# Optimization experiments

Hardware: AMD Instinct MI355X
Metric: run time of the kernel (lower is better)

Reference implementation:

```python
import jax, jax.numpy as jnp
import numpy as np

THRESHOLD = 0.1
EPS = 1e-06


def _bilinear_warp(img, flow):
    """Backward-warp img [B,1,H,W] by flow [B,2,H,W] with bilinear sampling,
    zero padding for out-of-range taps (F.grid_sample zeros-padding semantics)."""
    B, _, H, W = img.shape
    imgf = img[:, 0].reshape(B, H * W)                      # [B, H*W]
    ys, xs = jnp.meshgrid(jnp.arange(H, dtype=flow.dtype),
                          jnp.arange(W, dtype=flow.dtype), indexing='ij')
    x = xs[None] + flow[:, 0]                               # [B,H,W] sample x
    y = ys[None] + flow[:, 1]                               # [B,H,W] sample y
    x0 = jnp.floor(x)
    y0 = jnp.floor(y)
    wx = x - x0
    wy = y - y0
    x0i = x0.astype(jnp.int32)
    y0i = y0.astype(jnp.int32)

    def tap(xi, yi):
        inb = ((xi >= 0) & (xi < W) & (yi >= 0) & (yi < H)).astype(img.dtype)
        idx = (jnp.clip(yi, 0, H - 1) * W + jnp.clip(xi, 0, W - 1)).reshape(B, H * W)
        vals = jnp.take_along_axis(imgf, idx, axis=1).reshape(B, H, W)
        return vals * inb

    out = (tap(x0i, y0i) * (1 - wx) * (1 - wy)
           + tap(x0i + 1, y0i) * wx * (1 - wy)
           + tap(x0i, y0i + 1) * (1 - wx) * wy
           + tap(x0i + 1, y0i + 1) * wx * wy)
    return out[:, None]                                     # [B,1,H,W]


def _forward(img1, img2, flow, event_voxels, valid_mask):
    B, _, H, W = flow.shape
    C = event_voxels.shape[1]
    rgb_w = jnp.array([0.299, 0.587, 0.114], dtype=img1.dtype)
    gray1 = jnp.einsum('bchw,c->bhw', img1, rgb_w)[:, None]  # [B,1,H,W]
    gray2 = jnp.einsum('bchw,c->bhw', img2, rgb_w)[:, None]
    warped_gray2 = _bilinear_warp(gray2, flow)
    normalized_change = jnp.tanh((warped_gray2 - gray1) * 5.0)[:, 0]  # [B,H,W]
    pos = jax.nn.relu(normalized_change)
    neg = jax.nn.relu(-normalized_change)

    # pred_events: ch0=pos, ch1=neg, ch i+2 = pos*w + neg*(1-w), w=(i+1)/(C-1)
    rem = C - 2
    w = jnp.arange(1, rem + 1, dtype=pos.dtype) / (rem + 1)          # [rem]
    mix = pos[:, None] * w[None, :, None, None] + neg[:, None] * (1 - w)[None, :, None, None]
    pred_events = jnp.concatenate([pos[:, None], neg[:, None], mix], axis=1)  # [B,C,H,W]

    flow_mag = jnp.sqrt(flow[:, 0] ** 2 + flow[:, 1] ** 2)
    event_mask = (flow_mag > THRESHOLD).astype(flow.dtype)[:, None]  # [B,1,H,W]
    combined_mask = valid_mask * event_mask                          # broadcasts over C
    combined_mask = jnp.broadcast_to(combined_mask, pred_events.shape)

    mask_sum = combined_mask.sum() + EPS
    pred_m = pred_events * combined_mask
    gt_m = event_voxels * combined_mask
    l1_loss = jnp.abs(pred_m - gt_m).sum() / mask_sum

    # batched correlation over (b,c)
    pred_flat = pred_m.reshape(B, C, -1)
    gt_flat = gt_m.reshape(B, C, -1)
    pn = pred_flat - pred_flat.mean(axis=-1, keepdims=True)
    gn = gt_flat - gt_flat.mean(axis=-1, keepdims=True)
    num = (pn * gn).sum(axis=-1)                                     # [B,C]
    den = jnp.linalg.norm(pn, axis=-1) * jnp.linalg.norm(gn, axis=-1) + EPS
    corr = num / den
    valid = combined_mask.sum(axis=(2, 3)) > 0                        # [B,C]
    corr_loss = jnp.where(valid, 1.0 - corr, 0.0).sum() / (B * C)

    loss = l1_loss + 0.5 * corr_loss
    return loss, pred_events


def setup_inputs() -> dict:
    key = jax.random.key(0)
    k1, k2, k3, k4, k5 = jax.random.split(key, 5)
    B, H, W, C = 8, 480, 640, 5
    return {
        'img1': jax.random.uniform(k1, (B, 3, H, W), dtype=jnp.float32),
        'img2': jax.random.uniform(k2, (B, 3, H, W), dtype=jnp.float32),
        'flow': jax.random.normal(k3, (B, 2, H, W), dtype=jnp.float32),
        'event_voxels': jax.random.normal(k4, (B, C, H, W), dtype=jnp.float32),
        'valid_mask': jax.random.uniform(k5, (B, 1, H, W), dtype=jnp.float32),
    }


def reference(img1, img2, flow, event_voxels, valid_mask):
    return _forward(img1, img2, flow, event_voxels, valid_mask)
```

## Files before the change

### kernel.cpp

```cpp
#include <hip/hip_runtime.h>
#include <hip/hip_fp16.h>
#include <math.h>

#define BB 8
#define HH 480
#define WW 640
#define CC 5
#define HW (HH * WW)
#define NBLK 300
#define NST 21

#define PARTIAL_OFFSET 4096
#define GRAY2_OFFSET (PARTIAL_OFFSET + 2400 * 32 * 4)

__device__ __forceinline__ float fast_tanh5(float d) {
    float ez = __expf(-10.0f * d);
    return (1.0f - ez) * __builtin_amdgcn_rcpf(1.0f + ez);
}

__device__ __forceinline__ float mixc(int c, float pos, float neg) {
    if (c == 0) return pos;
    if (c == 1) return neg;
    const float w = 0.25f * (float)(c - 1);
    return w * pos + (1.0f - w) * neg;
}

__device__ __forceinline__ float wave_sum_dpp(float v) {
    v += __int_as_float(__builtin_amdgcn_update_dpp(0, __float_as_int(v), 0x111, 0xf, 0xf, false));
    v += __int_as_float(__builtin_amdgcn_update_dpp(0, __float_as_int(v), 0x112, 0xf, 0xf, false));
    v += __int_as_float(__builtin_amdgcn_update_dpp(0, __float_as_int(v), 0x114, 0xf, 0xf, false));
    v += __int_as_float(__builtin_amdgcn_update_dpp(0, __float_as_int(v), 0x118, 0xf, 0xf, false));
    v += __int_as_float(__builtin_amdgcn_update_dpp(0, __float_as_int(v), 0x142, 0xa, 0xf, false));
    v += __int_as_float(__builtin_amdgcn_update_dpp(0, __float_as_int(v), 0x143, 0xc, 0xf, false));
    return v;
}

__global__ __launch_bounds__(256) void k_gray2(const float* __restrict__ img2,
                                               __half* __restrict__ gray2h) {
    const int phys = blockIdx.x;
    const int b = phys & 7;
    const int j = phys >> 3;
    const int p8 = j * 2048 + threadIdx.x * 8;
    const float* src = img2 + (size_t)b * 3 * HW + p8;
    float4 r0 = *(const float4*)(src);
    float4 r1 = *(const float4*)(src + 4);
    float4 g0 = *(const float4*)(src + HW);
    float4 g1 = *(const float4*)(src + HW + 4);
    float4 b0 = *(const float4*)(src + 2 * HW);
    float4 b1 = *(const float4*)(src + 2 * HW + 4);
    __half o[8];
    o[0] = __float2half(0.299f * r0.x + 0.587f * g0.x + 0.114f * b0.x);
    o[1] = __float2half(0.299f * r0.y + 0.587f * g0.y + 0.114f * b0.y);
    o[2] = __float2half(0.299f * r0.z + 0.587f * g0.z + 0.114f * b0.z);
    o[3] = __float2half(0.299f * r0.w + 0.587f * g0.w + 0.114f * b0.w);
    o[4] = __float2half(0.299f * r1.x + 0.587f * g1.x + 0.114f * b1.x);
    o[5] = __float2half(0.299f * r1.y + 0.587f * g1.y + 0.114f * b1.y);
    o[6] = __float2half(0.299f * r1.z + 0.587f * g1.z + 0.114f * b1.z);
    o[7] = __float2half(0.299f * r1.w + 0.587f * g1.w + 0.114f * b1.w);
    *(uint4*)(gray2h + (size_t)b * HW + p8) = *(const uint4*)o;
}

__global__ __launch_bounds__(256, 2) void k_main(
    const float* __restrict__ img1, const float* __restrict__ flow,
    const float* __restrict__ ev, const float* __restrict__ vmask,
    const __half* __restrict__ gray2h, float* __restrict__ pred_out,
    float* __restrict__ partial)
{
    const int b  = blockIdx.x & 7;
    const int bx = blockIdx.x >> 3;
    const float* i1  = img1  + (size_t)b * 3 * HW;
    const float* fl  = flow  + (size_t)b * 2 * HW;
    const float* evb = ev    + (size_t)b * CC * HW;
    const float* vm  = vmask + (size_t)b * HW;
    const __half* g2 = gray2h + (size_t)b * HW;
    float* po = pred_out + (size_t)b * CC * HW;

    const int tid = threadIdx.x;
    const int P   = bx * 1024;
    const int p4  = P + 4 * tid;
    const int py  = p4 / WW;
    const int px0 = p4 - py * WW;

    __shared__ float sdata[4][NST];

    float4 fx4 = *(const float4*)(fl + p4);
    float4 fy4 = *(const float4*)(fl + HW + p4);

    float fxa[4] = { fx4.x, fx4.y, fx4.z, fx4.w };
    float fya[4] = { fy4.x, fy4.y, fy4.z, fy4.w };

    int   adr[16];
    float wgt[16];
#pragma unroll
    for (int j = 0; j < 4; ++j) {
        float fx = fxa[j], fy = fya[j];
        float x = (float)(px0 + j) + fx;
        float y = (float)py + fy;
        float x0f = floorf(x);
        float y0f = floorf(y);
        float wx = x - x0f;
        float wy = y - y0f;
        int x0 = (int)x0f, y0 = (int)y0f;
        int x1 = x0 + 1,   y1 = y0 + 1;
        int cx0 = min(max(x0, 0), WW - 1);
        int cx1 = min(max(x1, 0), WW - 1);
        int cy0 = min(max(y0, 0), HH - 1);
        int cy1 = min(max(y1, 0), HH - 1);
        float wx0 = (1.0f - wx) * ((x0 >= 0 && x0 < WW) ? 1.0f : 0.0f);
        float wx1 = wx          * ((x1 >= 0 && x1 < WW) ? 1.0f : 0.0f);
        float wy0 = (1.0f - wy) * ((y0 >= 0 && y0 < HH) ? 1.0f : 0.0f);
        float wy1 = wy          * ((y1 >= 0 && y1 < HH) ? 1.0f : 0.0f);
        adr[j*4+0] = cy0 * WW + cx0;
        adr[j*4+1] = cy0 * WW + cx1;
        adr[j*4+2] = cy1 * WW + cx0;
        adr[j*4+3] = cy1 * WW + cx1;
        wgt[j*4+0] = wx0 * wy0;
        wgt[j*4+1] = wx1 * wy0;
        wgt[j*4+2] = wx0 * wy1;
        wgt[j*4+3] = wx1 * wy1;
    }

    __half tvh[16];
#pragma unroll
    for (int t = 0; t < 16; ++t) tvh[t] = g2[adr[t]];

    float4 c0  = *(const float4*)(i1 + p4);
    float4 c1  = *(const float4*)(i1 + HW + p4);
    float4 c2  = *(const float4*)(i1 + 2 * HW + p4);
    float4 vm4 = *(const float4*)(vm + p4);
    float4 ev4[CC];
#pragma unroll
    for (int c = 0; c < CC; ++c) ev4[c] = *(const float4*)(evb + c * HW + p4);

    float g1a[4] = {
        0.299f * c0.x + 0.587f * c1.x + 0.114f * c2.x,
        0.299f * c0.y + 0.587f * c1.y + 0.114f * c2.y,
        0.299f * c0.z + 0.587f * c1.z + 0.114f * c2.z,
        0.299f * c0.w + 0.587f * c1.w + 0.114f * c2.w };
    float vma[4] = { vm4.x, vm4.y, vm4.z, vm4.w };

    float acc[NST];
#pragma unroll
    for (int i = 0; i < NST; ++i) acc[i] = 0.0f;

    float posA[4], negA[4], posmA[4], negmA[4], mA[4];

#pragma unroll
    for (int j = 0; j < 4; ++j) {
        float warp = __half2float(tvh[j*4+0]) * wgt[j*4+0]
                   + __half2float(tvh[j*4+1]) * wgt[j*4+1]
                   + __half2float(tvh[j*4+2]) * wgt[j*4+2]
                   + __half2float(tvh[j*4+3]) * wgt[j*4+3];

        float nc  = fast_tanh5(warp - g1a[j]);
        float pos = fmaxf(nc, 0.0f);
        float neg = fmaxf(-nc, 0.0f);
        posA[j] = pos;
        negA[j] = neg;

        float fx = fxa[j], fy = fya[j];
        float m = ((fx * fx + fy * fy) > 0.01f) ? vma[j] : 0.0f;
        mA[j] = m;
        float posm = pos * m;
        float negm = neg * m;
        posmA[j] = posm;
        negmA[j] = negm;
        acc[1] += m;
        acc[2] += posm;
        acc[3] += negm;
        acc[4] += posm * posm;
        acc[5] += negm * negm;
    }

#pragma unroll
    for (int c = 0; c < CC; ++c) {
        const float ga[4] = { ev4[c].x, ev4[c].y, ev4[c].z, ev4[c].w };
#pragma unroll
        for (int j = 0; j < 4; ++j) {
            float pm = mixc(c, posmA[j], negmA[j]);
            float gm = ga[j] * mA[j];
            acc[0]      += fabsf(pm - gm);
            acc[6 + c]  += gm;
            acc[11 + c] += gm * gm;
            acc[16 + c] += pm * gm;
        }
    }

    const int lane = tid & 63;
    float npos[3], nneg[3];
#pragma unroll
    for (int j = 0; j < 3; ++j) {
        npos[j] = __shfl_down(posA[j], 1, 64);
        nneg[j] = __shfl_down(negA[j], 1, 64);
    }

#pragma unroll
    for (int c = 0; c < CC; ++c) {
        float* ob = po + c * HW + P + 4 * tid;
        if (lane < 63) {
            float4 v;
            v.x = mixc(c, posA[3], negA[3]);
            v.y = mixc(c, npos[0], nneg[0]);
            v.z = mixc(c, npos[1], nneg[1]);
            v.w = mixc(c, npos[2], nneg[2]);
            *(float4*)(ob + 3) = v;
        } else {
            ob[3] = mixc(c, posA[3], negA[3]);
        }
        if (lane == 0) {
            ob[0] = mixc(c, posA[0], negA[0]);
            ob[1] = mixc(c, posA[1], negA[1]);
            ob[2] = mixc(c, posA[2], negA[2]);
        }
    }

    const int wid = tid >> 6;
#pragma unroll
    for (int i = 0; i < NST; ++i) acc[i] = wave_sum_dpp(acc[i]);
    if (lane == 63) {
#pragma unroll
        for (int i = 0; i < NST; ++i) sdata[wid][i] = acc[i];
    }

    __syncthreads();

    if (tid < NST) {
        float s = sdata[0][tid] + sdata[1][tid] + sdata[2][tid] + sdata[3][tid];
        partial[(size_t)(b * NBLK + bx) * 32 + tid] = s;
    }
}

__global__ void k_reduce(const float* __restrict__ partial, double* __restrict__ stats) {
    int bi = blockIdx.x;
    int b = bi / NST;
    int i = bi - b * NST;
    int t = threadIdx.x;
    double s = 0.0;
    for (int k = t; k < NBLK; k += 64)
        s += (double)partial[(size_t)(b * NBLK + k) * 32 + i];
    for (int off = 32; off > 0; off >>= 1) s += __shfl_down(s, off, 64);
    if (t == 0) stats[b * NST + i] = s;
}

__global__ void k_final(const double* __restrict__ stats, float* __restrict__ out) {
    int t = threadIdx.x;
    double contrib = 0.0;
    if (t < BB * CC) {
        int b = t / CC;
        int c = t - b * CC;
        const double* s = stats + b * NST;
        const double wA[CC] = { 1.0, 0.0, 0.25, 0.50, 0.75 };
        const double wB[CC] = { 0.0, 1.0, 0.75, 0.50, 0.25 };
        double a = wA[c], bb = wB[c];
        double Sp  = a * s[2] + bb * s[3];
        double Spp = a * a * s[4] + bb * bb * s[5];
        double Sg  = s[6 + c];
        double Sgg = s[11 + c];
        double Spg = s[16 + c];
        const double N = (double)HW;
        double num  = Spg - Sp * Sg / N;
        double varp = Spp - Sp * Sp / N; if (varp < 0.0) varp = 0.0;
        double varg = Sgg - Sg * Sg / N; if (varg < 0.0) varg = 0.0;
        double den  = sqrt(varp) * sqrt(varg) + 1e-6;
        double corr = num / den;
        bool valid = s[1] > 0.0;
        contrib = valid ? (1.0 - corr) : 0.0;
    }
    for (int off = 32; off > 0; off >>= 1) contrib += __shfl_down(contrib, off, 64);
    if (t == 0) {
        double msum_total = 0.0, l1sum = 0.0;
        for (int b = 0; b < BB; ++b) {
            msum_total += stats[b * NST + 1];
            l1sum      += stats[b * NST + 0];
        }
        double mask_sum = (double)CC * msum_total + 1e-6;
        double l1_loss = l1sum / mask_sum;
        double corr_loss = contrib / (double)(BB * CC);
        out[0] = (float)(l1_loss + 0.5 * corr_loss);
    }
}

extern "C" void kernel_launch(void* const* d_in, const int* in_sizes, int n_in,
                              void* d_out, int out_size, void* d_ws, size_t ws_size,
                              hipStream_t stream) {
    const float* img1  = (const float*)d_in[0];
    const float* img2  = (const float*)d_in[1];
    const float* flow  = (const float*)d_in[2];
    const float* ev    = (const float*)d_in[3];
    const float* vmask = (const float*)d_in[4];
    float* out = (float*)d_out;

    double* stats   = (double*)d_ws;
    float*  partial = (float*)((char*)d_ws + PARTIAL_OFFSET);
    __half* gray2h  = (__half*)((char*)d_ws + GRAY2_OFFSET);

    k_gray2<<<1200, 256, 0, stream>>>(img2, gray2h);

    k_main<<<2400, 256, 0, stream>>>(img1, flow, ev, vmask, gray2h, out + 1, partial);

    k_reduce<<<BB * NST, 64, 0, stream>>>(partial, stats);

    k_final<<<1, 64, 0, stream>>>(stats, out);
}
```

Baseline: 42.90 us.

## Store horizontally paired gray2 texels as half2 to halve warp gathers

Measured after the change: 44.56 us. 3.9% more time.

```diff
diff --git a/kernel.cpp b/kernel.cpp
--- a/kernel.cpp
+++ b/kernel.cpp
@@ -36,34 +36,45 @@
 }
 
 __global__ __launch_bounds__(256) void k_gray2(const float* __restrict__ img2,
-                                               __half* __restrict__ gray2h) {
+                                               __half2* __restrict__ qb) {
     const int phys = blockIdx.x;
     const int b = phys & 7;
     const int j = phys >> 3;
     const int p8 = j * 2048 + threadIdx.x * 8;
-    const float* src = img2 + (size_t)b * 3 * HW + p8;
+    const float* i2 = img2 + (size_t)b * 3 * HW;
+    const float* src = i2 + p8;
     float4 r0 = *(const float4*)(src);
     float4 r1 = *(const float4*)(src + 4);
     float4 g0 = *(const float4*)(src + HW);
     float4 g1 = *(const float4*)(src + HW + 4);
     float4 b0 = *(const float4*)(src + 2 * HW);
     float4 b1 = *(const float4*)(src + 2 * HW + 4);
-    __half o[8];
-    o[0] = __float2half(0.299f * r0.x + 0.587f * g0.x + 0.114f * b0.x);
-    o[1] = __float2half(0.299f * r0.y + 0.587f * g0.y + 0.114f * b0.y);
-    o[2] = __float2half(0.299f * r0.z + 0.587f * g0.z + 0.114f * b0.z);
-    o[3] = __float2half(0.299f * r0.w + 0.587f * g0.w + 0.114f * b0.w);
-    o[4] = __float2half(0.299f * r1.x + 0.587f * g1.x + 0.114f * b1.x);
-    o[5] = __float2half(0.299f * r1.y + 0.587f * g1.y + 0.114f * b1.y);
-    o[6] = __float2half(0.299f * r1.z + 0.587f * g1.z + 0.114f * b1.z);
-    o[7] = __float2half(0.299f * r1.w + 0.587f * g1.w + 0.114f * b1.w);
-    *(uint4*)(gray2h + (size_t)b * HW + p8) = *(const uint4*)o;
+    const int o9 = min(p8 + 8, HW - 1);
+    float r8 = i2[o9], g8 = i2[o9 + HW], b8 = i2[o9 + 2 * HW];
+
+    float gr[9];
+    gr[0] = 0.299f * r0.x + 0.587f * g0.x + 0.114f * b0.x;
+    gr[1] = 0.299f * r0.y + 0.587f * g0.y + 0.114f * b0.y;
+    gr[2] = 0.299f * r0.z + 0.587f * g0.z + 0.114f * b0.z;
+    gr[3] = 0.299f * r0.w + 0.587f * g0.w + 0.114f * b0.w;
+    gr[4] = 0.299f * r1.x + 0.587f * g1.x + 0.114f * b1.x;
+    gr[5] = 0.299f * r1.y + 0.587f * g1.y + 0.114f * b1.y;
+    gr[6] = 0.299f * r1.z + 0.587f * g1.z + 0.114f * b1.z;
+    gr[7] = 0.299f * r1.w + 0.587f * g1.w + 0.114f * b1.w;
+    gr[8] = 0.299f * r8   + 0.587f * g8   + 0.114f * b8;
+
+    __half2 o[8];
+#pragma unroll
+    for (int k = 0; k < 8; ++k) o[k] = __floats2half2_rn(gr[k], gr[k + 1]);
+    __half2* dst = qb + (size_t)b * HW + p8;
+    *(uint4*)(dst)     = *(const uint4*)(&o[0]);
+    *(uint4*)(dst + 4) = *(const uint4*)(&o[4]);
 }
 
 __global__ __launch_bounds__(256, 2) void k_main(
     const float* __restrict__ img1, const float* __restrict__ flow,
     const float* __restrict__ ev, const float* __restrict__ vmask,
-    const __half* __restrict__ gray2h, float* __restrict__ pred_out,
+    const __half2* __restrict__ qb, float* __restrict__ pred_out,
     float* __restrict__ partial)
 {
     const int b  = blockIdx.x & 7;
@@ -72,7 +83,7 @@
     const float* fl  = flow  + (size_t)b * 2 * HW;
     const float* evb = ev    + (size_t)b * CC * HW;
     const float* vm  = vmask + (size_t)b * HW;
-    const __half* g2 = gray2h + (size_t)b * HW;
+    const __half2* g2p = qb + (size_t)b * HW;
     float* po = pred_out + (size_t)b * CC * HW;
 
     const int tid = threadIdx.x;
@@ -89,8 +100,8 @@
     float fxa[4] = { fx4.x, fx4.y, fx4.z, fx4.w };
     float fya[4] = { fy4.x, fy4.y, fy4.z, fy4.w };
 
-    int   adr[16];
-    float wgt[16];
+    int   adrA[4], adrB[4];
+    float wxA[4], wxB[4], wyA[4], wyB[4];
 #pragma unroll
     for (int j = 0; j < 4; ++j) {
         float fx = fxa[j], fy = fya[j];
@@ -101,28 +112,23 @@
         float wx = x - x0f;
         float wy = y - y0f;
         int x0 = (int)x0f, y0 = (int)y0f;
-        int x1 = x0 + 1,   y1 = y0 + 1;
-        int cx0 = min(max(x0, 0), WW - 1);
-        int cx1 = min(max(x1, 0), WW - 1);
+        int y1 = y0 + 1;
+        int b0 = min(max(x0, 0), WW - 2);
         int cy0 = min(max(y0, 0), HH - 1);
         int cy1 = min(max(y1, 0), HH - 1);
-        float wx0 = (1.0f - wx) * ((x0 >= 0 && x0 < WW) ? 1.0f : 0.0f);
-        float wx1 = wx          * ((x1 >= 0 && x1 < WW) ? 1.0f : 0.0f);
-        float wy0 = (1.0f - wy) * ((y0 >= 0 && y0 < HH) ? 1.0f : 0.0f);
-        float wy1 = wy          * ((y1 >= 0 && y1 < HH) ? 1.0f : 0.0f);
-        adr[j*4+0] = cy0 * WW + cx0;
-        adr[j*4+1] = cy0 * WW + cx1;
-        adr[j*4+2] = cy1 * WW + cx0;
-        adr[j*4+3] = cy1 * WW + cx1;
-        wgt[j*4+0] = wx0 * wy0;
-        wgt[j*4+1] = wx1 * wy0;
-        wgt[j*4+2] = wx0 * wy1;
-        wgt[j*4+3] = wx1 * wy1;
-    }
-
-    __half tvh[16];
-#pragma unroll
-    for (int t = 0; t < 16; ++t) tvh[t] = g2[adr[t]];
+        wxA[j] = (b0 == x0) ? (1.0f - wx) : ((x0 == -1) ? wx : 0.0f);
+        wxB[j] = (b0 == x0) ? wx : ((b0 + 1 == x0) ? (1.0f - wx) : 0.0f);
+        wyA[j] = (1.0f - wy) * ((y0 >= 0 && y0 < HH) ? 1.0f : 0.0f);
+        wyB[j] = wy          * ((y1 >= 0 && y1 < HH) ? 1.0f : 0.0f);
+        adrA[j] = cy0 * WW + b0;
+        adrB[j] = cy1 * WW + b0;
+    }
+
+    __half2 qa[4], qbv[4];
+#pragma unroll
+    for (int j = 0; j < 4; ++j) qa[j]  = g2p[adrA[j]];
+#pragma unroll
+    for (int j = 0; j < 4; ++j) qbv[j] = g2p[adrB[j]];
 
     float4 c0  = *(const float4*)(i1 + p4);
     float4 c1  = *(const float4*)(i1 + HW + p4);
@@ -147,10 +153,9 @@
 
 #pragma unroll
     for (int j = 0; j < 4; ++j) {
-        float warp = __half2float(tvh[j*4+0]) * wgt[j*4+0]
-                   + __half2float(tvh[j*4+1]) * wgt[j*4+1]
-                   + __half2float(tvh[j*4+2]) * wgt[j*4+2]
-                   + __half2float(tvh[j*4+3]) * wgt[j*4+3];
+        float rowT = wxA[j] * __low2float(qa[j])  + wxB[j] * __high2float(qa[j]);
+        float rowB = wxA[j] * __low2float(qbv[j]) + wxB[j] * __high2float(qbv[j]);
+        float warp = wyA[j] * rowT + wyB[j] * rowB;
 
         float nc  = fast_tanh5(warp - g1a[j]);
         float pos = fmaxf(nc, 0.0f);
@@ -290,13 +295,13 @@
     const float* vmask = (const float*)d_in[4];
     float* out = (float*)d_out;
 
-    double* stats   = (double*)d_ws;
-    float*  partial = (float*)((char*)d_ws + PARTIAL_OFFSET);
-    __half* gray2h  = (__half*)((char*)d_ws + GRAY2_OFFSET);
-
-    k_gray2<<<1200, 256, 0, stream>>>(img2, gray2h);
-
-    k_main<<<2400, 256, 0, stream>>>(img1, flow, ev, vmask, gray2h, out + 1, partial);
+    double*  stats   = (double*)d_ws;
+    float*   partial = (float*)((char*)d_ws + PARTIAL_OFFSET);
+    __half2* qbuf    = (__half2*)((char*)d_ws + GRAY2_OFFSET);
+
+    k_gray2<<<1200, 256, 0, stream>>>(img2, qbuf);
+
+    k_main<<<2400, 256, 0, stream>>>(img1, flow, ev, vmask, qbuf, out + 1, partial);
 
     k_reduce<<<BB * NST, 64, 0, stream>>>(partial, stats);
 
```

## Loop main kernel over four tiles per block and merge reduce/final kernels

Applied to the files above, without the earlier changes.

Result: slower. 46.74 us (+9.0%).

```diff
diff --git a/kernel.cpp b/kernel.cpp
--- a/kernel.cpp
+++ b/kernel.cpp
@@ -7,7 +7,8 @@
 #define WW 640
 #define CC 5
 #define HW (HH * WW)
-#define NBLK 300
+#define NBLKB 75
+#define NTILE 4
 #define NST 21
 
 #define PARTIAL_OFFSET 4096
@@ -67,7 +68,7 @@
     float* __restrict__ partial)
 {
     const int b  = blockIdx.x & 7;
-    const int bx = blockIdx.x >> 3;
+    const int j0 = blockIdx.x >> 3;
     const float* i1  = img1  + (size_t)b * 3 * HW;
     const float* fl  = flow  + (size_t)b * 2 * HW;
     const float* evb = ev    + (size_t)b * CC * HW;
@@ -75,146 +76,157 @@
     const __half* g2 = gray2h + (size_t)b * HW;
     float* po = pred_out + (size_t)b * CC * HW;
 
-    const int tid = threadIdx.x;
-    const int P   = bx * 1024;
-    const int p4  = P + 4 * tid;
-    const int py  = p4 / WW;
-    const int px0 = p4 - py * WW;
+    const int tid  = threadIdx.x;
+    const int lane = tid & 63;
+    const int wid  = tid >> 6;
 
     __shared__ float sdata[4][NST];
 
-    float4 fx4 = *(const float4*)(fl + p4);
-    float4 fy4 = *(const float4*)(fl + HW + p4);
-
-    float fxa[4] = { fx4.x, fx4.y, fx4.z, fx4.w };
-    float fya[4] = { fy4.x, fy4.y, fy4.z, fy4.w };
-
-    int   adr[16];
-    float wgt[16];
-#pragma unroll
-    for (int j = 0; j < 4; ++j) {
-        float fx = fxa[j], fy = fya[j];
-        float x = (float)(px0 + j) + fx;
-        float y = (float)py + fy;
-        float x0f = floorf(x);
-        float y0f = floorf(y);
-        float wx = x - x0f;
-        float wy = y - y0f;
-        int x0 = (int)x0f, y0 = (int)y0f;
-        int x1 = x0 + 1,   y1 = y0 + 1;
-        int cx0 = min(max(x0, 0), WW - 1);
-        int cx1 = min(max(x1, 0), WW - 1);
-        int cy0 = min(max(y0, 0), HH - 1);
-        int cy1 = min(max(y1, 0), HH - 1);
-        float wx0 = (1.0f - wx) * ((x0 >= 0 && x0 < WW) ? 1.0f : 0.0f);
-        float wx1 = wx          * ((x1 >= 0 && x1 < WW) ? 1.0f : 0.0f);
-        float wy0 = (1.0f - wy) * ((y0 >= 0 && y0 < HH) ? 1.0f : 0.0f);
-        float wy1 = wy          * ((y1 >= 0 && y1 < HH) ? 1.0f : 0.0f);
-        adr[j*4+0] = cy0 * WW + cx0;
-        adr[j*4+1] = cy0 * WW + cx1;
-        adr[j*4+2] = cy1 * WW + cx0;
-        adr[j*4+3] = cy1 * WW + cx1;
-        wgt[j*4+0] = wx0 * wy0;
-        wgt[j*4+1] = wx1 * wy0;
-        wgt[j*4+2] = wx0 * wy1;
-        wgt[j*4+3] = wx1 * wy1;
-    }
-
-    __half tvh[16];
-#pragma unroll
-    for (int t = 0; t < 16; ++t) tvh[t] = g2[adr[t]];
-
-    float4 c0  = *(const float4*)(i1 + p4);
-    float4 c1  = *(const float4*)(i1 + HW + p4);
-    float4 c2  = *(const float4*)(i1 + 2 * HW + p4);
-    float4 vm4 = *(const float4*)(vm + p4);
-    float4 ev4[CC];
-#pragma unroll
-    for (int c = 0; c < CC; ++c) ev4[c] = *(const float4*)(evb + c * HW + p4);
-
-    float g1a[4] = {
-        0.299f * c0.x + 0.587f * c1.x + 0.114f * c2.x,
-        0.299f * c0.y + 0.587f * c1.y + 0.114f * c2.y,
-        0.299f * c0.z + 0.587f * c1.z + 0.114f * c2.z,
-        0.299f * c0.w + 0.587f * c1.w + 0.114f * c2.w };
-    float vma[4] = { vm4.x, vm4.y, vm4.z, vm4.w };
-
     float acc[NST];
 #pragma unroll
     for (int i = 0; i < NST; ++i) acc[i] = 0.0f;
 
-    float posA[4], negA[4], posmA[4], negmA[4], mA[4];
-
-#pragma unroll
-    for (int j = 0; j < 4; ++j) {
-        float warp = __half2float(tvh[j*4+0]) * wgt[j*4+0]
-                   + __half2float(tvh[j*4+1]) * wgt[j*4+1]
-                   + __half2float(tvh[j*4+2]) * wgt[j*4+2]
-                   + __half2float(tvh[j*4+3]) * wgt[j*4+3];
-
-        float nc  = fast_tanh5(warp - g1a[j]);
-        float pos = fmaxf(nc, 0.0f);
-        float neg = fmaxf(-nc, 0.0f);
-        posA[j] = pos;
-        negA[j] = neg;
-
-        float fx = fxa[j], fy = fya[j];
-        float m = ((fx * fx + fy * fy) > 0.01f) ? vma[j] : 0.0f;
-        mA[j] = m;
-        float posm = pos * m;
-        float negm = neg * m;
-        posmA[j] = posm;
-        negmA[j] = negm;
-        acc[1] += m;
-        acc[2] += posm;
-        acc[3] += negm;
-        acc[4] += posm * posm;
-        acc[5] += negm * negm;
-    }
-
-#pragma unroll
-    for (int c = 0; c < CC; ++c) {
-        const float ga[4] = { ev4[c].x, ev4[c].y, ev4[c].z, ev4[c].w };
+    int P = j0 * 1024;
+    float4 fx4 = *(const float4*)(fl + P + 4 * tid);
+    float4 fy4 = *(const float4*)(fl + HW + P + 4 * tid);
+
+    for (int t = 0; t < NTILE; ++t) {
+        const int p4  = P + 4 * tid;
+        const int py  = p4 / WW;
+        const int px0 = p4 - py * WW;
+
+        float fxa[4] = { fx4.x, fx4.y, fx4.z, fx4.w };
+        float fya[4] = { fy4.x, fy4.y, fy4.z, fy4.w };
+
+        int   adr[16];
+        float wgt[16];
 #pragma unroll
         for (int j = 0; j < 4; ++j) {
-            float pm = mixc(c, posmA[j], negmA[j]);
-            float gm = ga[j] * mA[j];
-            acc[0]      += fabsf(pm - gm);
-            acc[6 + c]  += gm;
-            acc[11 + c] += gm * gm;
-            acc[16 + c] += pm * gm;
-        }
-    }
-
-    const int lane = tid & 63;
-    float npos[3], nneg[3];
-#pragma unroll
-    for (int j = 0; j < 3; ++j) {
-        npos[j] = __shfl_down(posA[j], 1, 64);
-        nneg[j] = __shfl_down(negA[j], 1, 64);
-    }
-
-#pragma unroll
-    for (int c = 0; c < CC; ++c) {
-        float* ob = po + c * HW + P + 4 * tid;
-        if (lane < 63) {
-            float4 v;
-            v.x = mixc(c, posA[3], negA[3]);
-            v.y = mixc(c, npos[0], nneg[0]);
-            v.z = mixc(c, npos[1], nneg[1]);
-            v.w = mixc(c, npos[2], nneg[2]);
-            *(float4*)(ob + 3) = v;
-        } else {
-            ob[3] = mixc(c, posA[3], negA[3]);
-        }
-        if (lane == 0) {
-            ob[0] = mixc(c, posA[0], negA[0]);
-            ob[1] = mixc(c, posA[1], negA[1]);
-            ob[2] = mixc(c, posA[2], negA[2]);
-        }
-    }
-
-    const int wid = tid >> 6;
+            float fx = fxa[j], fy = fya[j];
+            float x = (float)(px0 + j) + fx;
+            float y = (float)py + fy;
+            float x0f = floorf(x);
+            float y0f = floorf(y);
+            float wx = x - x0f;
+            float wy = y - y0f;
+            int x0 = (int)x0f, y0 = (int)y0f;
+            int x1 = x0 + 1,   y1 = y0 + 1;
+            int cx0 = min(max(x0, 0), WW - 1);
+            int cx1 = min(max(x1, 0), WW - 1);
+            int cy0 = min(max(y0, 0), HH - 1);
+            int cy1 = min(max(y1, 0), HH - 1);
+            float wx0 = (1.0f - wx) * ((x0 >= 0 && x0 < WW) ? 1.0f : 0.0f);
+            float wx1 = wx          * ((x1 >= 0 && x1 < WW) ? 1.0f : 0.0f);
+            float wy0 = (1.0f - wy) * ((y0 >= 0 && y0 < HH) ? 1.0f : 0.0f);
+            float wy1 = wy          * ((y1 >= 0 && y1 < HH) ? 1.0f : 0.0f);
+            adr[j*4+0] = cy0 * WW + cx0;
+            adr[j*4+1] = cy0 * WW + cx1;
+            adr[j*4+2] = cy1 * WW + cx0;
+            adr[j*4+3] = cy1 * WW + cx1;
+            wgt[j*4+0] = wx0 * wy0;
+            wgt[j*4+1] = wx1 * wy0;
+            wgt[j*4+2] = wx0 * wy1;
+            wgt[j*4+3] = wx1 * wy1;
+        }
+
+        __half tvh[16];
+#pragma unroll
+        for (int k = 0; k < 16; ++k) tvh[k] = g2[adr[k]];
+
+        float4 c0  = *(const float4*)(i1 + p4);
+        float4 c1  = *(const float4*)(i1 + HW + p4);
+        float4 c2  = *(const float4*)(i1 + 2 * HW + p4);
+        float4 vm4 = *(const float4*)(vm + p4);
+        float4 ev4[CC];
+#pragma unroll
+        for (int c = 0; c < CC; ++c) ev4[c] = *(const float4*)(evb + c * HW + p4);
+
+        const int Pn = P + NBLKB * 1024;
+        if (t + 1 < NTILE) {
+            fx4 = *(const float4*)(fl + Pn + 4 * tid);
+            fy4 = *(const float4*)(fl + HW + Pn + 4 * tid);
+        }
+
+        float g1a[4] = {
+            0.299f * c0.x + 0.587f * c1.x + 0.114f * c2.x,
+            0.299f * c0.y + 0.587f * c1.y + 0.114f * c2.y,
+            0.299f * c0.z + 0.587f * c1.z + 0.114f * c2.z,
+            0.299f * c0.w + 0.587f * c1.w + 0.114f * c2.w };
+        float vma[4] = { vm4.x, vm4.y, vm4.z, vm4.w };
+
+        float posA[4], negA[4], posmA[4], negmA[4], mA[4];
+
+#pragma unroll
+        for (int j = 0; j < 4; ++j) {
+            float warp = __half2float(tvh[j*4+0]) * wgt[j*4+0]
+                       + __half2float(tvh[j*4+1]) * wgt[j*4+1]
+                       + __half2float(tvh[j*4+2]) * wgt[j*4+2]
+                       + __half2float(tvh[j*4+3]) * wgt[j*4+3];
+
+            float nc  = fast_tanh5(warp - g1a[j]);
+            float pos = fmaxf(nc, 0.0f);
+            float neg = fmaxf(-nc, 0.0f);
+            posA[j] = pos;
+            negA[j] = neg;
+
+            float fx = fxa[j], fy = fya[j];
+            float m = ((fx * fx + fy * fy) > 0.01f) ? vma[j] : 0.0f;
+            mA[j] = m;
+            float posm = pos * m;
+            float negm = neg * m;
+            posmA[j] = posm;
+            negmA[j] = negm;
+            acc[1] += m;
+            acc[2] += posm;
+            acc[3] += negm;
+            acc[4] += posm * posm;
+            acc[5] += negm * negm;
+        }
+
+#pragma unroll
+        for (int c = 0; c < CC; ++c) {
+            const float ga[4] = { ev4[c].x, ev4[c].y, ev4[c].z, ev4[c].w };
+#pragma unroll
+            for (int j = 0; j < 4; ++j) {
+                float pm = mixc(c, posmA[j], negmA[j]);
+                float gm = ga[j] * mA[j];
+                acc[0]      += fabsf(pm - gm);
+                acc[6 + c]  += gm;
+                acc[11 + c] += gm * gm;
+                acc[16 + c] += pm * gm;
+            }
+        }
+
+        float npos[3], nneg[3];
+#pragma unroll
+        for (int j = 0; j < 3; ++j) {
+            npos[j] = __shfl_down(posA[j], 1, 64);
+            nneg[j] = __shfl_down(negA[j], 1, 64);
+        }
+
+#pragma unroll
+        for (int c = 0; c < CC; ++c) {
+            float* ob = po + c * HW + p4;
+            if (lane < 63) {
+                float4 v;
+                v.x = mixc(c, posA[3], negA[3]);
+                v.y = mixc(c, npos[0], nneg[0]);
+                v.z = mixc(c, npos[1], nneg[1]);
+                v.w = mixc(c, npos[2], nneg[2]);
+                *(float4*)(ob + 3) = v;
+            } else {
+                ob[3] = mixc(c, posA[3], negA[3]);
+            }
+            if (lane == 0) {
+                ob[0] = mixc(c, posA[0], negA[0]);
+                ob[1] = mixc(c, posA[1], negA[1]);
+                ob[2] = mixc(c, posA[2], negA[2]);
+            }
+        }
+
+        P = Pn;
+    }
+
 #pragma unroll
     for (int i = 0; i < NST; ++i) acc[i] = wave_sum_dpp(acc[i]);
     if (lane == 63) {
@@ -226,29 +238,29 @@
 
     if (tid < NST) {
         float s = sdata[0][tid] + sdata[1][tid] + sdata[2][tid] + sdata[3][tid];
-        partial[(size_t)(b * NBLK + bx) * 32 + tid] = s;
-    }
-}
-
-__global__ void k_reduce(const float* __restrict__ partial, double* __restrict__ stats) {
-    int bi = blockIdx.x;
-    int b = bi / NST;
-    int i = bi - b * NST;
-    int t = threadIdx.x;
-    double s = 0.0;
-    for (int k = t; k < NBLK; k += 64)
-        s += (double)partial[(size_t)(b * NBLK + k) * 32 + i];
-    for (int off = 32; off > 0; off >>= 1) s += __shfl_down(s, off, 64);
-    if (t == 0) stats[b * NST + i] = s;
-}
-
-__global__ void k_final(const double* __restrict__ stats, float* __restrict__ out) {
-    int t = threadIdx.x;
-    double contrib = 0.0;
+        partial[(size_t)(b * NBLKB + j0) * 32 + tid] = s;
+    }
+}
+
+__global__ void k_fin(const float* __restrict__ partial, float* __restrict__ out) {
+    __shared__ double sums[BB][NST];
+    __shared__ double contribs[BB * CC];
+    const int t = threadIdx.x;
+
+    if (t < BB * NST) {
+        int b = t / NST;
+        int i = t - b * NST;
+        double s = 0.0;
+        for (int k = 0; k < NBLKB; ++k)
+            s += (double)partial[(size_t)(b * NBLKB + k) * 32 + i];
+        sums[b][i] = s;
+    }
+    __syncthreads();
+
     if (t < BB * CC) {
         int b = t / CC;
         int c = t - b * CC;
-        const double* s = stats + b * NST;
+        const double* s = sums[b];
         const double wA[CC] = { 1.0, 0.0, 0.25, 0.50, 0.75 };
         const double wB[CC] = { 0.0, 1.0, 0.75, 0.50, 0.25 };
         double a = wA[c], bb = wB[c];
@@ -264,19 +276,16 @@
         double den  = sqrt(varp) * sqrt(varg) + 1e-6;
         double corr = num / den;
         bool valid = s[1] > 0.0;
-        contrib = valid ? (1.0 - corr) : 0.0;
-    }
-    for (int off = 32; off > 0; off >>= 1) contrib += __shfl_down(contrib, off, 64);
+        contribs[t] = valid ? (1.0 - corr) : 0.0;
+    }
+    __syncthreads();
+
     if (t == 0) {
-        double msum_total = 0.0, l1sum = 0.0;
-        for (int b = 0; b < BB; ++b) {
-            msum_total += stats[b * NST + 1];
-            l1sum      += stats[b * NST + 0];
-        }
-        double mask_sum = (double)CC * msum_total + 1e-6;
-        double l1_loss = l1sum / mask_sum;
-        double corr_loss = contrib / (double)(BB * CC);
-        out[0] = (float)(l1_loss + 0.5 * corr_loss);
+        double msum = 0.0, l1sum = 0.0, csum = 0.0;
+        for (int b = 0; b < BB; ++b) { msum += sums[b][1]; l1sum += sums[b][0]; }
+        for (int i = 0; i < BB * CC; ++i) csum += contribs[i];
+        double mask_sum = (double)CC * msum + 1e-6;
+        out[0] = (float)(l1sum / mask_sum + 0.5 * (csum / (double)(BB * CC)));
     }
 }
 
@@ -290,15 +299,12 @@
     const float* vmask = (const float*)d_in[4];
     float* out = (float*)d_out;
 
-    double* stats   = (double*)d_ws;
     float*  partial = (float*)((char*)d_ws + PARTIAL_OFFSET);
     __half* gray2h  = (__half*)((char*)d_ws + GRAY2_OFFSET);
 
     k_gray2<<<1200, 256, 0, stream>>>(img2, gray2h);
 
-    k_main<<<2400, 256, 0, stream>>>(img1, flow, ev, vmask, gray2h, out + 1, partial);
-
-    k_reduce<<<BB * NST, 64, 0, stream>>>(partial, stats);
-
-    k_final<<<1, 64, 0, stream>>>(stats, out);
-}
+    k_main<<<600, 256, 0, stream>>>(img1, flow, ev, vmask, gray2h, out + 1, partial);
+
+    k_fin<<<1, 256, 0, stream>>>(partial, out);
+}
```
